# Kernel optimization log

Hardware: AMD Instinct MI355X
Metric: run time of the kernel (lower is better)

Reference implementation:

```python
import jax, jax.numpy as jnp
import numpy as np

HEAD_DIM = 128
PROJ_DIM = 64


def setup_inputs() -> dict:
    key = jax.random.key(0)
    kq, kk, kv, kr = jax.random.split(key, 4)
    B, H, NQ, NKV = 1, 16, 2048, 4096
    Q = jax.random.normal(kq, (B, H, NQ, HEAD_DIM), dtype=jnp.float32)
    K = jax.random.normal(kk, (B, H, NKV, HEAD_DIM), dtype=jnp.float32)
    V = jax.random.normal(kv, (B, H, NKV, HEAD_DIM), dtype=jnp.float32)
    # R ~ N(0,1) / sqrt(proj_dim), as in the torch __init__
    R = jax.random.normal(kr, (HEAD_DIM, PROJ_DIM), dtype=jnp.float32) / (PROJ_DIM ** 0.5)
    return {"Q": Q, "K": K, "V": V, "R": R}


def reference(Q, K, V, R):
    proj_dim = R.shape[-1]
    scale = 1.0 / (proj_dim ** 0.5)
    # Project Q and K into the random-projection space: [B,H,N,proj_dim]
    Q_proj = jnp.einsum('bhnd,dp->bhnp', Q, R)
    K_proj = jnp.einsum('bhmd,dp->bhmp', K, R)
    # scores: [B,H,NQ,NKV]
    scores = jnp.einsum('bhnp,bhmp->bhnm', Q_proj, K_proj) * scale
    weights = jax.nn.softmax(scores, axis=-1)
    # output: [B,H,NQ,head_dim]
    return jnp.einsum('bhnm,bhmd->bhnd', weights, V)
```

## Files before the change

kernel.cpp:

```cpp
#include <hip/hip_runtime.h>

#define HEADS 16
#define NQ    2048
#define NKV   4096
#define DH    128
#define PDIM  64

typedef __bf16 bf16_t;
typedef bf16_t bf16x8 __attribute__((ext_vector_type(8)));
typedef bf16_t bf16x4 __attribute__((ext_vector_type(4)));
typedef bf16_t bf16x2 __attribute__((ext_vector_type(2)));
typedef float  f32x4  __attribute__((ext_vector_type(4)));
typedef float  f32x16 __attribute__((ext_vector_type(16)));
typedef int    i32x4  __attribute__((ext_vector_type(4)));

typedef __attribute__((address_space(3))) unsigned int       lds_u32;
typedef __attribute__((address_space(1))) const unsigned int glb_u32;

__device__ __forceinline__ void dma16(const void* g, void* l) {
  __builtin_amdgcn_global_load_lds((glb_u32*)g, (lds_u32*)l, 16, 0, 0);
}

__global__ __launch_bounds__(256) void proj_kernel(
    const float* __restrict__ Q, const float* __restrict__ K,
    const float* __restrict__ R, bf16_t* __restrict__ Qp, bf16_t* __restrict__ Kp)
{
  __shared__ bf16_t sY[4][16 * 72];
  const int tid  = threadIdx.x;
  const int wave = tid >> 6, lane = tid & 63;
  const int n16  = lane & 15, quad = lane >> 4;

  bf16x8 bfr[4][4];
#pragma unroll
  for (int nt = 0; nt < 4; ++nt) {
    const int n = nt * 16 + n16;
#pragma unroll
    for (int kk = 0; kk < 4; ++kk) {
      const int k0 = kk * 32 + quad * 8;
      bf16x8 b;
#pragma unroll
      for (int j = 0; j < 8; ++j) b[j] = (bf16_t)R[(k0 + j) * PDIM + n];
      bfr[nt][kk] = b;
    }
  }

  const long rowblock = (long)blockIdx.x * 256 + wave * 64;
  const long qrows = (long)HEADS * NQ;

#pragma unroll 1
  for (int t = 0; t < 4; ++t) {
    const long r0 = rowblock + t * 16;
    const float* X; bf16_t* Y; float scale; long xrow;
    if (r0 < qrows) { X = Q; Y = Qp; scale = 0.18033688011112042f; xrow = r0; }
    else            { X = K; Y = Kp; scale = 1.0f;                 xrow = r0 - qrows; }

    const float* xp = X + (xrow + n16) * DH;
    bf16x8 a[4];
#pragma unroll
    for (int kk = 0; kk < 4; ++kk) {
      const int k0 = kk * 32 + quad * 8;
      f32x4 x0 = *(const f32x4*)(xp + k0);
      f32x4 x1 = *(const f32x4*)(xp + k0 + 4);
      bf16x8 av;
#pragma unroll
      for (int j = 0; j < 4; ++j) { av[j] = (bf16_t)(x0[j] * scale); av[4 + j] = (bf16_t)(x1[j] * scale); }
      a[kk] = av;
    }
    bf16_t* sy = sY[wave];
#pragma unroll
    for (int nt = 0; nt < 4; ++nt) {
      f32x4 acc = {0.f, 0.f, 0.f, 0.f};
#pragma unroll
      for (int kk = 0; kk < 4; ++kk)
        acc = __builtin_amdgcn_mfma_f32_16x16x32_bf16(a[kk], bfr[nt][kk], acc, 0, 0, 0);
#pragma unroll
      for (int r = 0; r < 4; ++r)
        sy[(quad * 4 + r) * 72 + nt * 16 + n16] = (bf16_t)acc[r];
    }
    const int row = lane >> 2, cg = lane & 3;
    bf16x8 w0 = *(const bf16x8*)(&sy[row * 72 + cg * 16]);
    bf16x8 w1 = *(const bf16x8*)(&sy[row * 72 + cg * 16 + 8]);
    *(bf16x8*)(Y + (xrow + row) * PDIM + cg * 16)     = w0;
    *(bf16x8*)(Y + (xrow + row) * PDIM + cg * 16 + 8) = w1;
  }
}

__global__ __launch_bounds__(256) void vtrans_kernel(
    const float* __restrict__ V, bf16_t* __restrict__ Vt)
{
  __shared__ float sF[64 * 129];
  const int tid = threadIdx.x;
  const int h = blockIdx.y, jt = blockIdx.x;
  const float* vp = V + ((long)h * NKV + jt * 64) * DH;
#pragma unroll
  for (int rep = 0; rep < 8; ++rep) {
    const int slot = tid + rep * 256;
    const int j = slot >> 5, c4 = (slot & 31) * 4;
    f32x4 v = *(const f32x4*)(vp + j * DH + c4);
    float* dst = &sF[j * 129 + c4];
    dst[0] = v[0]; dst[1] = v[1]; dst[2] = v[2]; dst[3] = v[3];
  }
  __syncthreads();
  bf16_t* op = Vt + (long)h * DH * NKV + jt * 64;
#pragma unroll
  for (int rep = 0; rep < 4; ++rep) {
    const int slot = tid + rep * 256;
    const int d = slot >> 3, j8 = (slot & 7) * 8;
    bf16x8 w;
#pragma unroll
    for (int jj = 0; jj < 8; ++jj) w[jj] = (bf16_t)sF[(j8 + jj) * 129 + d];
    *(bf16x8*)(op + (long)d * NKV + j8) = w;
  }
}

__global__ __launch_bounds__(128, 2) void flash_kernel(
    const bf16_t* __restrict__ Qp, const bf16_t* __restrict__ Kp,
    const bf16_t* __restrict__ Vt, bf16_t* __restrict__ Opart,
    float* __restrict__ Lpart, float* __restrict__ Out,
    int splits, int iters)
{
  __shared__ char smem[24576];
  bf16_t* sK = (bf16_t*)smem;
  bf16_t* sV = (bf16_t*)(smem + 8192);

  const int tid  = threadIdx.x;
  const int wave = tid >> 6, lane = tid & 63;
  const int l31  = lane & 31, h = lane >> 5;

  const int head = blockIdx.x & 15;
  const int qt   = (blockIdx.x >> 4) & 15;
  const int sp   = blockIdx.x >> 8;

  const int qbase = qt * 128 + wave * 64;
  const int kv0   = sp * (64 * iters);

  bf16x8 qf[2][4];
#pragma unroll
  for (int qsub = 0; qsub < 2; ++qsub)
#pragma unroll
    for (int k = 0; k < 4; ++k)
      qf[qsub][k] = *(const bf16x8*)(Qp + ((long)head * NQ + qbase + qsub * 32 + l31) * PDIM
                                     + k * 16 + h * 8);

  f32x16 o[2][4] = {};
  float rsum[2] = {0.f, 0.f};

  const bf16_t* kpH = Kp + (long)head * NKV * PDIM;
  const bf16_t* vtH = Vt + (long)head * DH * NKV;

  const int sw = ((lane & 7) ^ ((lane >> 3) & 7)) * 8;
  const int r8 = lane >> 3;

  for (int t = 0; t < iters; ++t) {
    const int kvb = kv0 + t * 64;
    __syncthreads();
    if (wave == 0) {
#pragma unroll
      for (int i = 0; i < 8; ++i)
        dma16(kpH + (long)(kvb + i * 8 + r8) * PDIM + sw, smem + i * 1024);
#pragma unroll
      for (int i = 0; i < 4; ++i)
        dma16(vtH + (long)(i * 8 + r8) * NKV + kvb + sw, smem + 8192 + i * 1024);
    } else {
#pragma unroll
      for (int i = 4; i < 16; ++i)
        dma16(vtH + (long)(i * 8 + r8) * NKV + kvb + sw, smem + 8192 + i * 1024);
    }
    __syncthreads();

#pragma unroll
    for (int s = 0; s < 2; ++s) {
      int bfr[2][2][4];
#pragma unroll
      for (int qsub = 0; qsub < 2; ++qsub) {
        f32x16 sc = {};
        const int r = s * 32 + l31;
#pragma unroll
        for (int k = 0; k < 4; ++k) {
          const int c = 2 * k + h;
          const bf16x8 a = *(const bf16x8*)(sK + r * 64 + ((c ^ (r & 7)) * 8));
          sc = __builtin_amdgcn_mfma_f32_32x32x16_bf16(a, qf[qsub][k], sc, 0, 0, 0);
        }
        int pk[4][2];
#pragma unroll
        for (int rg = 0; rg < 4; ++rg) {
          const float p0 = __builtin_amdgcn_exp2f(sc[rg * 4 + 0]);
          const float p1 = __builtin_amdgcn_exp2f(sc[rg * 4 + 1]);
          const float p2 = __builtin_amdgcn_exp2f(sc[rg * 4 + 2]);
          const float p3 = __builtin_amdgcn_exp2f(sc[rg * 4 + 3]);
          rsum[qsub] += (p0 + p1) + (p2 + p3);
          union { bf16x2 v; int i; } u0, u1;
          u0.v = bf16x2{(bf16_t)p0, (bf16_t)p1};
          u1.v = bf16x2{(bf16_t)p2, (bf16_t)p3};
          pk[rg][0] = u0.i; pk[rg][1] = u1.i;
        }
#pragma unroll
        for (int cl = 0; cl < 2; ++cl) {
          const int e00 = __shfl_xor(pk[2 * cl][0], 32);
          const int e01 = __shfl_xor(pk[2 * cl][1], 32);
          const int e10 = __shfl_xor(pk[2 * cl + 1][0], 32);
          const int e11 = __shfl_xor(pk[2 * cl + 1][1], 32);
          bfr[qsub][cl][0] = h ? e10 : pk[2 * cl][0];
          bfr[qsub][cl][1] = h ? e11 : pk[2 * cl][1];
          bfr[qsub][cl][2] = h ? pk[2 * cl + 1][0] : e00;
          bfr[qsub][cl][3] = h ? pk[2 * cl + 1][1] : e01;
        }
      }
#pragma unroll
      for (int dsub = 0; dsub < 4; ++dsub) {
        const int r = dsub * 32 + l31;
#pragma unroll
        for (int cl = 0; cl < 2; ++cl) {
          const int c = 2 * (2 * s + cl) + h;
          const bf16x8 va = *(const bf16x8*)(sV + r * 64 + ((c ^ (r & 7)) * 8));
#pragma unroll
          for (int qsub = 0; qsub < 2; ++qsub) {
            union { i32x4 i; bf16x8 v; } pb;
            pb.i = i32x4{bfr[qsub][cl][0], bfr[qsub][cl][1],
                         bfr[qsub][cl][2], bfr[qsub][cl][3]};
            o[qsub][dsub] = __builtin_amdgcn_mfma_f32_32x32x16_bf16(va, pb.v, o[qsub][dsub], 0, 0, 0);
          }
        }
      }
    }
  }

  __syncthreads();
  bf16_t* myT = (bf16_t*)(smem + wave * 8704);
#pragma unroll
  for (int qsub = 0; qsub < 2; ++qsub) {
    const float lsum = rsum[qsub] + __shfl_xor(rsum[qsub], 32);
    const float scale = (splits > 1) ? 1.0f : (1.0f / lsum);
#pragma unroll
    for (int dsub = 0; dsub < 4; ++dsub)
#pragma unroll
      for (int rg = 0; rg < 4; ++rg) {
        bf16x4 w = { (bf16_t)(o[qsub][dsub][rg * 4 + 0] * scale),
                     (bf16_t)(o[qsub][dsub][rg * 4 + 1] * scale),
                     (bf16_t)(o[qsub][dsub][rg * 4 + 2] * scale),
                     (bf16_t)(o[qsub][dsub][rg * 4 + 3] * scale) };
        *(bf16x4*)(myT + l31 * 136 + dsub * 32 + rg * 8 + h * 4) = w;
      }
    const int qglob = qbase + qsub * 32;
#pragma unroll
    for (int j = 0; j < 8; ++j) {
      const int ql = j * 4 + (lane >> 4);
      bf16x8 v = *(const bf16x8*)(myT + ql * 136 + (lane & 15) * 8);
      if (splits > 1) {
        *(bf16x8*)(Opart + (((long)sp * HEADS + head) * NQ + qglob + ql) * DH + (lane & 15) * 8) = v;
      } else {
        float* op = Out + ((long)head * NQ + qglob + ql) * DH + (lane & 15) * 8;
        f32x4 a = {(float)v[0], (float)v[1], (float)v[2], (float)v[3]};
        f32x4 b = {(float)v[4], (float)v[5], (float)v[6], (float)v[7]};
        *(f32x4*)op = a; *(f32x4*)(op + 4) = b;
      }
    }
    if (splits > 1 && h == 0)
      Lpart[((long)sp * HEADS + head) * NQ + qglob + l31] = lsum;
  }
}

__global__ __launch_bounds__(256) void combine_kernel(
    const bf16_t* __restrict__ Opart, const float* __restrict__ Lpart,
    float* __restrict__ Out)
{
  const long idx = (long)blockIdx.x * 256 + threadIdx.x;
  const int  d8  = (int)(idx & 15);
  const long hq  = idx >> 4;
  float l = 0.f;
  float acc[8];
#pragma unroll
  for (int j = 0; j < 8; ++j) acc[j] = 0.f;
#pragma unroll
  for (int s = 0; s < 4; ++s) {
    l += Lpart[s * (long)(HEADS * NQ) + hq];
    bf16x8 v = *(const bf16x8*)(Opart + (s * (long)(HEADS * NQ) + hq) * DH + d8 * 8);
#pragma unroll
    for (int j = 0; j < 8; ++j) acc[j] += (float)v[j];
  }
  const float inv = 1.f / l;
  f32x4 o0 = { acc[0] * inv, acc[1] * inv, acc[2] * inv, acc[3] * inv };
  f32x4 o1 = { acc[4] * inv, acc[5] * inv, acc[6] * inv, acc[7] * inv };
  float* op = Out + hq * DH + d8 * 8;
  *(f32x4*)(op)     = o0;
  *(f32x4*)(op + 4) = o1;
}

extern "C" void kernel_launch(void* const* d_in, const int* in_sizes, int n_in,
                              void* d_out, int out_size, void* d_ws, size_t ws_size,
                              hipStream_t stream)
{
  const float* Q = (const float*)d_in[0];
  const float* K = (const float*)d_in[1];
  const float* V = (const float*)d_in[2];
  const float* R = (const float*)d_in[3];
  float* Out = (float*)d_out;

  char* ws = (char*)d_ws;
  bf16_t* Qp = (bf16_t*)(ws);
  bf16_t* Kp = (bf16_t*)(ws + (size_t)(4  << 20));
  bf16_t* Vt = (bf16_t*)(ws + (size_t)(12 << 20));
  bf16_t* Opart = (bf16_t*)(ws + (size_t)(28 << 20));
  float*  Lpart = (float*)(ws + (size_t)(60 << 20));

  const size_t need4 = (size_t)(60 << 20) + 4ull * HEADS * NQ * sizeof(float);
  const int splits = (ws_size >= need4) ? 4 : 1;
  const int iters  = NKV / (64 * splits);

  proj_kernel<<<384, 256, 0, stream>>>(Q, K, R, Qp, Kp);
  vtrans_kernel<<<dim3(64, 16), 256, 0, stream>>>(V, Vt);
  flash_kernel<<<splits * 256, 128, 0, stream>>>(Qp, Kp, Vt, Opart, Lpart, Out,
                                                 splits, iters);
  if (splits == 4)
    combine_kernel<<<2048, 256, 0, stream>>>(Opart, Lpart, Out);
}
```

Before: 203.6 us.

## Double-buffer K/V tiles, merge prep kernels, use three uneven KV splits

```diff
diff --git a/kernel.cpp b/kernel.cpp
--- a/kernel.cpp
+++ b/kernel.cpp
@@ -21,107 +21,105 @@
   __builtin_amdgcn_global_load_lds((glb_u32*)g, (lds_u32*)l, 16, 0, 0);
 }
 
-__global__ __launch_bounds__(256) void proj_kernel(
+__global__ __launch_bounds__(256) void prep_kernel(
     const float* __restrict__ Q, const float* __restrict__ K,
-    const float* __restrict__ R, bf16_t* __restrict__ Qp, bf16_t* __restrict__ Kp)
+    const float* __restrict__ V, const float* __restrict__ R,
+    bf16_t* __restrict__ Qp, bf16_t* __restrict__ Kp, bf16_t* __restrict__ Vt)
 {
-  __shared__ bf16_t sY[4][16 * 72];
-  const int tid  = threadIdx.x;
-  const int wave = tid >> 6, lane = tid & 63;
-  const int n16  = lane & 15, quad = lane >> 4;
-
-  bf16x8 bfr[4][4];
-#pragma unroll
-  for (int nt = 0; nt < 4; ++nt) {
-    const int n = nt * 16 + n16;
-#pragma unroll
-    for (int kk = 0; kk < 4; ++kk) {
-      const int k0 = kk * 32 + quad * 8;
-      bf16x8 b;
-#pragma unroll
-      for (int j = 0; j < 8; ++j) b[j] = (bf16_t)R[(k0 + j) * PDIM + n];
-      bfr[nt][kk] = b;
-    }
-  }
-
-  const long rowblock = (long)blockIdx.x * 256 + wave * 64;
-  const long qrows = (long)HEADS * NQ;
+  __shared__ char smem_raw[33024 * 4 > 36864 ? 33024 * 4 / 1 : 36864];
+  const int tid = threadIdx.x;
+
+  if (blockIdx.x < 384) {
+    bf16_t* sY = (bf16_t*)smem_raw;
+    const int wave = tid >> 6, lane = tid & 63;
+    const int n16  = lane & 15, quad = lane >> 4;
+
+    bf16x8 bfr[4][4];
+#pragma unroll
+    for (int nt = 0; nt < 4; ++nt) {
+      const int n = nt * 16 + n16;
+#pragma unroll
+      for (int kk = 0; kk < 4; ++kk) {
+        const int k0 = kk * 32 + quad * 8;
+        bf16x8 b;
+#pragma unroll
+        for (int j = 0; j < 8; ++j) b[j] = (bf16_t)R[(k0 + j) * PDIM + n];
+        bfr[nt][kk] = b;
+      }
+    }
+
+    const long rowblock = (long)blockIdx.x * 256 + wave * 64;
+    const long qrows = (long)HEADS * NQ;
 
 #pragma unroll 1
-  for (int t = 0; t < 4; ++t) {
-    const long r0 = rowblock + t * 16;
-    const float* X; bf16_t* Y; float scale; long xrow;
-    if (r0 < qrows) { X = Q; Y = Qp; scale = 0.18033688011112042f; xrow = r0; }
-    else            { X = K; Y = Kp; scale = 1.0f;                 xrow = r0 - qrows; }
-
-    const float* xp = X + (xrow + n16) * DH;
-    bf16x8 a[4];
-#pragma unroll
-    for (int kk = 0; kk < 4; ++kk) {
-      const int k0 = kk * 32 + quad * 8;
-      f32x4 x0 = *(const f32x4*)(xp + k0);
-      f32x4 x1 = *(const f32x4*)(xp + k0 + 4);
-      bf16x8 av;
-#pragma unroll
-      for (int j = 0; j < 4; ++j) { av[j] = (bf16_t)(x0[j] * scale); av[4 + j] = (bf16_t)(x1[j] * scale); }
-      a[kk] = av;
-    }
-    bf16_t* sy = sY[wave];
-#pragma unroll
-    for (int nt = 0; nt < 4; ++nt) {
-      f32x4 acc = {0.f, 0.f, 0.f, 0.f};
-#pragma unroll
-      for (int kk = 0; kk < 4; ++kk)
-        acc = __builtin_amdgcn_mfma_f32_16x16x32_bf16(a[kk], bfr[nt][kk], acc, 0, 0, 0);
-#pragma unroll
-      for (int r = 0; r < 4; ++r)
-        sy[(quad * 4 + r) * 72 + nt * 16 + n16] = (bf16_t)acc[r];
-    }
-    const int row = lane >> 2, cg = lane & 3;
-    bf16x8 w0 = *(const bf16x8*)(&sy[row * 72 + cg * 16]);
-    bf16x8 w1 = *(const bf16x8*)(&sy[row * 72 + cg * 16 + 8]);
-    *(bf16x8*)(Y + (xrow + row) * PDIM + cg * 16)     = w0;
-    *(bf16x8*)(Y + (xrow + row) * PDIM + cg * 16 + 8) = w1;
-  }
-}
-
-__global__ __launch_bounds__(256) void vtrans_kernel(
-    const float* __restrict__ V, bf16_t* __restrict__ Vt)
-{
-  __shared__ float sF[64 * 129];
-  const int tid = threadIdx.x;
-  const int h = blockIdx.y, jt = blockIdx.x;
-  const float* vp = V + ((long)h * NKV + jt * 64) * DH;
-#pragma unroll
-  for (int rep = 0; rep < 8; ++rep) {
-    const int slot = tid + rep * 256;
-    const int j = slot >> 5, c4 = (slot & 31) * 4;
-    f32x4 v = *(const f32x4*)(vp + j * DH + c4);
-    float* dst = &sF[j * 129 + c4];
-    dst[0] = v[0]; dst[1] = v[1]; dst[2] = v[2]; dst[3] = v[3];
-  }
-  __syncthreads();
-  bf16_t* op = Vt + (long)h * DH * NKV + jt * 64;
-#pragma unroll
-  for (int rep = 0; rep < 4; ++rep) {
-    const int slot = tid + rep * 256;
-    const int d = slot >> 3, j8 = (slot & 7) * 8;
-    bf16x8 w;
-#pragma unroll
-    for (int jj = 0; jj < 8; ++jj) w[jj] = (bf16_t)sF[(j8 + jj) * 129 + d];
-    *(bf16x8*)(op + (long)d * NKV + j8) = w;
+    for (int t = 0; t < 4; ++t) {
+      const long r0 = rowblock + t * 16;
+      const float* X; bf16_t* Y; float scale; long xrow;
+      if (r0 < qrows) { X = Q; Y = Qp; scale = 0.18033688011112042f; xrow = r0; }
+      else            { X = K; Y = Kp; scale = 1.0f;                 xrow = r0 - qrows; }
+
+      const float* xp = X + (xrow + n16) * DH;
+      bf16x8 a[4];
+#pragma unroll
+      for (int kk = 0; kk < 4; ++kk) {
+        const int k0 = kk * 32 + quad * 8;
+        f32x4 x0 = *(const f32x4*)(xp + k0);
+        f32x4 x1 = *(const f32x4*)(xp + k0 + 4);
+        bf16x8 av;
+#pragma unroll
+        for (int j = 0; j < 4; ++j) { av[j] = (bf16_t)(x0[j] * scale); av[4 + j] = (bf16_t)(x1[j] * scale); }
+        a[kk] = av;
+      }
+      bf16_t* sy = sY + wave * (16 * 72);
+#pragma unroll
+      for (int nt = 0; nt < 4; ++nt) {
+        f32x4 acc = {0.f, 0.f, 0.f, 0.f};
+#pragma unroll
+        for (int kk = 0; kk < 4; ++kk)
+          acc = __builtin_amdgcn_mfma_f32_16x16x32_bf16(a[kk], bfr[nt][kk], acc, 0, 0, 0);
+#pragma unroll
+        for (int r = 0; r < 4; ++r)
+          sy[(quad * 4 + r) * 72 + nt * 16 + n16] = (bf16_t)acc[r];
+      }
+      const int row = lane >> 2, cg = lane & 3;
+      bf16x8 w0 = *(const bf16x8*)(&sy[row * 72 + cg * 16]);
+      bf16x8 w1 = *(const bf16x8*)(&sy[row * 72 + cg * 16 + 8]);
+      *(bf16x8*)(Y + (xrow + row) * PDIM + cg * 16)     = w0;
+      *(bf16x8*)(Y + (xrow + row) * PDIM + cg * 16 + 8) = w1;
+    }
+  } else {
+    float* sF = (float*)smem_raw;
+    const int bid = blockIdx.x - 384;
+    const int h = bid >> 6, jt = bid & 63;
+    const float* vp = V + ((long)h * NKV + jt * 64) * DH;
+#pragma unroll
+    for (int rep = 0; rep < 8; ++rep) {
+      const int slot = tid + rep * 256;
+      const int j = slot >> 5, c4 = (slot & 31) * 4;
+      f32x4 v = *(const f32x4*)(vp + j * DH + c4);
+      float* dst = &sF[j * 129 + c4];
+      dst[0] = v[0]; dst[1] = v[1]; dst[2] = v[2]; dst[3] = v[3];
+    }
+    __syncthreads();
+    bf16_t* op = Vt + (long)h * DH * NKV + jt * 64;
+#pragma unroll
+    for (int rep = 0; rep < 4; ++rep) {
+      const int slot = tid + rep * 256;
+      const int d = slot >> 3, j8 = (slot & 7) * 8;
+      bf16x8 w;
+#pragma unroll
+      for (int jj = 0; jj < 8; ++jj) w[jj] = (bf16_t)sF[(j8 + jj) * 129 + d];
+      *(bf16x8*)(op + (long)d * NKV + j8) = w;
+    }
   }
 }
 
 __global__ __launch_bounds__(128, 2) void flash_kernel(
     const bf16_t* __restrict__ Qp, const bf16_t* __restrict__ Kp,
     const bf16_t* __restrict__ Vt, bf16_t* __restrict__ Opart,
-    float* __restrict__ Lpart, float* __restrict__ Out,
-    int splits, int iters)
+    float* __restrict__ Lpart, float* __restrict__ Out, int splits)
 {
-  __shared__ char smem[24576];
-  bf16_t* sK = (bf16_t*)smem;
-  bf16_t* sV = (bf16_t*)(smem + 8192);
+  __shared__ char smem[49152];
 
   const int tid  = threadIdx.x;
   const int wave = tid >> 6, lane = tid & 63;
@@ -132,7 +130,33 @@
   const int sp   = blockIdx.x >> 8;
 
   const int qbase = qt * 128 + wave * 64;
-  const int kv0   = sp * (64 * iters);
+  int n_t, t0;
+  if (splits == 3) { n_t = (sp == 0) ? 22 : 21; t0 = (sp == 0) ? 0 : 22 + 21 * (sp - 1); }
+  else             { n_t = 64; t0 = 0; }
+
+  const bf16_t* kpH = Kp + (long)head * NKV * PDIM;
+  const bf16_t* vtH = Vt + (long)head * DH * NKV;
+
+  const int sw = ((lane & 7) ^ ((lane >> 3) & 7)) * 8;
+  const int r8 = lane >> 3;
+
+  auto stage = [&](int t, char* buf) {
+    const int kvb = (t0 + t) * 64;
+    if (wave == 0) {
+#pragma unroll
+      for (int i = 0; i < 8; ++i)
+        dma16(kpH + (long)(kvb + i * 8 + r8) * PDIM + sw, buf + i * 1024);
+#pragma unroll
+      for (int i = 0; i < 4; ++i)
+        dma16(vtH + (long)(i * 8 + r8) * NKV + kvb + sw, buf + 8192 + i * 1024);
+    } else {
+#pragma unroll
+      for (int i = 4; i < 16; ++i)
+        dma16(vtH + (long)(i * 8 + r8) * NKV + kvb + sw, buf + 8192 + i * 1024);
+    }
+  };
+
+  stage(0, smem);
 
   bf16x8 qf[2][4];
 #pragma unroll
@@ -145,28 +169,13 @@
   f32x16 o[2][4] = {};
   float rsum[2] = {0.f, 0.f};
 
-  const bf16_t* kpH = Kp + (long)head * NKV * PDIM;
-  const bf16_t* vtH = Vt + (long)head * DH * NKV;
-
-  const int sw = ((lane & 7) ^ ((lane >> 3) & 7)) * 8;
-  const int r8 = lane >> 3;
-
-  for (int t = 0; t < iters; ++t) {
-    const int kvb = kv0 + t * 64;
+  for (int t = 0; t < n_t; ++t) {
     __syncthreads();
-    if (wave == 0) {
-#pragma unroll
-      for (int i = 0; i < 8; ++i)
-        dma16(kpH + (long)(kvb + i * 8 + r8) * PDIM + sw, smem + i * 1024);
-#pragma unroll
-      for (int i = 0; i < 4; ++i)
-        dma16(vtH + (long)(i * 8 + r8) * NKV + kvb + sw, smem + 8192 + i * 1024);
-    } else {
-#pragma unroll
-      for (int i = 4; i < 16; ++i)
-        dma16(vtH + (long)(i * 8 + r8) * NKV + kvb + sw, smem + 8192 + i * 1024);
-    }
-    __syncthreads();
+    if (t + 1 < n_t) stage(t + 1, smem + ((t + 1) & 1) * 24576);
+
+    char* cur = smem + (t & 1) * 24576;
+    bf16_t* sK = (bf16_t*)cur;
+    bf16_t* sV = (bf16_t*)(cur + 8192);
 
 #pragma unroll
     for (int s = 0; s < 2; ++s) {
@@ -262,7 +271,7 @@
 
 __global__ __launch_bounds__(256) void combine_kernel(
     const bf16_t* __restrict__ Opart, const float* __restrict__ Lpart,
-    float* __restrict__ Out)
+    float* __restrict__ Out, int splits)
 {
   const long idx = (long)blockIdx.x * 256 + threadIdx.x;
   const int  d8  = (int)(idx & 15);
@@ -271,8 +280,8 @@
   float acc[8];
 #pragma unroll
   for (int j = 0; j < 8; ++j) acc[j] = 0.f;
-#pragma unroll
-  for (int s = 0; s < 4; ++s) {
+#pragma unroll 1
+  for (int s = 0; s < splits; ++s) {
     l += Lpart[s * (long)(HEADS * NQ) + hq];
     bf16x8 v = *(const bf16x8*)(Opart + (s * (long)(HEADS * NQ) + hq) * DH + d8 * 8);
 #pragma unroll
@@ -301,16 +310,13 @@
   bf16_t* Kp = (bf16_t*)(ws + (size_t)(4  << 20));
   bf16_t* Vt = (bf16_t*)(ws + (size_t)(12 << 20));
   bf16_t* Opart = (bf16_t*)(ws + (size_t)(28 << 20));
-  float*  Lpart = (float*)(ws + (size_t)(60 << 20));
-
-  const size_t need4 = (size_t)(60 << 20) + 4ull * HEADS * NQ * sizeof(float);
-  const int splits = (ws_size >= need4) ? 4 : 1;
-  const int iters  = NKV / (64 * splits);
-
-  proj_kernel<<<384, 256, 0, stream>>>(Q, K, R, Qp, Kp);
-  vtrans_kernel<<<dim3(64, 16), 256, 0, stream>>>(V, Vt);
-  flash_kernel<<<splits * 256, 128, 0, stream>>>(Qp, Kp, Vt, Opart, Lpart, Out,
-                                                 splits, iters);
-  if (splits == 4)
-    combine_kernel<<<2048, 256, 0, stream>>>(Opart, Lpart, Out);
-}
+  float*  Lpart = (float*)(ws + (size_t)(52 << 20));
+
+  const size_t need3 = (size_t)(52 << 20) + 3ull * HEADS * NQ * sizeof(float);
+  const int splits = (ws_size >= need3) ? 3 : 1;
+
+  prep_kernel<<<1408, 256, 0, stream>>>(Q, K, V, R, Qp, Kp, Vt);
+  flash_kernel<<<splits * 256, 128, 0, stream>>>(Qp, Kp, Vt, Opart, Lpart, Out, splits);
+  if (splits == 3)
+    combine_kernel<<<2048, 256, 0, stream>>>(Opart, Lpart, Out, splits);
+}
```

Measured after the change: 262.9 us. 1.29x slower.

## Merge Q/K projection and V transpose into one prep kernel

Applied to the files above, without the earlier changes.

```diff
diff --git a/kernel.cpp b/kernel.cpp
--- a/kernel.cpp
+++ b/kernel.cpp
@@ -21,14 +21,54 @@
   __builtin_amdgcn_global_load_lds((glb_u32*)g, (lds_u32*)l, 16, 0, 0);
 }
 
-__global__ __launch_bounds__(256) void proj_kernel(
+__global__ __launch_bounds__(256) void prep_kernel(
     const float* __restrict__ Q, const float* __restrict__ K,
-    const float* __restrict__ R, bf16_t* __restrict__ Qp, bf16_t* __restrict__ Kp)
+    const float* __restrict__ V, const float* __restrict__ R,
+    bf16_t* __restrict__ Qp, bf16_t* __restrict__ Kp, bf16_t* __restrict__ Vt)
 {
+  __shared__ float  sF[64 * 132];
   __shared__ bf16_t sY[4][16 * 72];
-  const int tid  = threadIdx.x;
+  const int tid = threadIdx.x;
+  const int bid = blockIdx.x;
+
+  const int isQ = (bid < 512);
+  const int isK = (bid >= 512) && (bid < 1536);
+
+  const float* src;
+  long row0;
+  if (isQ)      { src = Q; row0 = (long)bid * 64; }
+  else if (isK) { src = K; row0 = (long)(bid - 512) * 64; }
+  else          { src = V; row0 = (long)(bid - 1536) * 64; }
+  const float* tp = src + row0 * DH;
+#pragma unroll
+  for (int rep = 0; rep < 8; ++rep) {
+    const int slot = tid + rep * 256;
+    const int j = slot >> 5, c4 = (slot & 31) * 4;
+    f32x4 v = *(const f32x4*)(tp + j * DH + c4);
+    *(f32x4*)(&sF[j * 132 + c4]) = v;
+  }
+  __syncthreads();
+
+  if (!isQ && !isK) {
+    const int vb = bid - 1536;
+    const int h = vb >> 6, jt = vb & 63;
+    bf16_t* op = Vt + (long)h * DH * NKV + jt * 64;
+#pragma unroll
+    for (int rep = 0; rep < 4; ++rep) {
+      const int slot = tid + rep * 256;
+      const int d = slot >> 3, j8 = (slot & 7) * 8;
+      bf16x8 w;
+#pragma unroll
+      for (int jj = 0; jj < 8; ++jj) w[jj] = (bf16_t)sF[(j8 + jj) * 132 + d];
+      *(bf16x8*)(op + (long)d * NKV + j8) = w;
+    }
+    return;
+  }
+
   const int wave = tid >> 6, lane = tid & 63;
   const int n16  = lane & 15, quad = lane >> 4;
+  const float scale = isQ ? 0.18033688011112042f : 1.0f;
+  bf16_t* Y = isQ ? Qp : Kp;
 
   bf16x8 bfr[4][4];
 #pragma unroll
@@ -44,73 +84,36 @@
     }
   }
 
-  const long rowblock = (long)blockIdx.x * 256 + wave * 64;
-  const long qrows = (long)HEADS * NQ;
-
-#pragma unroll 1
-  for (int t = 0; t < 4; ++t) {
-    const long r0 = rowblock + t * 16;
-    const float* X; bf16_t* Y; float scale; long xrow;
-    if (r0 < qrows) { X = Q; Y = Qp; scale = 0.18033688011112042f; xrow = r0; }
-    else            { X = K; Y = Kp; scale = 1.0f;                 xrow = r0 - qrows; }
-
-    const float* xp = X + (xrow + n16) * DH;
-    bf16x8 a[4];
-#pragma unroll
-    for (int kk = 0; kk < 4; ++kk) {
-      const int k0 = kk * 32 + quad * 8;
-      f32x4 x0 = *(const f32x4*)(xp + k0);
-      f32x4 x1 = *(const f32x4*)(xp + k0 + 4);
-      bf16x8 av;
-#pragma unroll
-      for (int j = 0; j < 4; ++j) { av[j] = (bf16_t)(x0[j] * scale); av[4 + j] = (bf16_t)(x1[j] * scale); }
-      a[kk] = av;
-    }
-    bf16_t* sy = sY[wave];
-#pragma unroll
-    for (int nt = 0; nt < 4; ++nt) {
-      f32x4 acc = {0.f, 0.f, 0.f, 0.f};
-#pragma unroll
-      for (int kk = 0; kk < 4; ++kk)
-        acc = __builtin_amdgcn_mfma_f32_16x16x32_bf16(a[kk], bfr[nt][kk], acc, 0, 0, 0);
-#pragma unroll
-      for (int r = 0; r < 4; ++r)
-        sy[(quad * 4 + r) * 72 + nt * 16 + n16] = (bf16_t)acc[r];
-    }
-    const int row = lane >> 2, cg = lane & 3;
-    bf16x8 w0 = *(const bf16x8*)(&sy[row * 72 + cg * 16]);
-    bf16x8 w1 = *(const bf16x8*)(&sy[row * 72 + cg * 16 + 8]);
-    *(bf16x8*)(Y + (xrow + row) * PDIM + cg * 16)     = w0;
-    *(bf16x8*)(Y + (xrow + row) * PDIM + cg * 16 + 8) = w1;
-  }
-}
-
-__global__ __launch_bounds__(256) void vtrans_kernel(
-    const float* __restrict__ V, bf16_t* __restrict__ Vt)
-{
-  __shared__ float sF[64 * 129];
-  const int tid = threadIdx.x;
-  const int h = blockIdx.y, jt = blockIdx.x;
-  const float* vp = V + ((long)h * NKV + jt * 64) * DH;
-#pragma unroll
-  for (int rep = 0; rep < 8; ++rep) {
-    const int slot = tid + rep * 256;
-    const int j = slot >> 5, c4 = (slot & 31) * 4;
-    f32x4 v = *(const f32x4*)(vp + j * DH + c4);
-    float* dst = &sF[j * 129 + c4];
-    dst[0] = v[0]; dst[1] = v[1]; dst[2] = v[2]; dst[3] = v[3];
-  }
-  __syncthreads();
-  bf16_t* op = Vt + (long)h * DH * NKV + jt * 64;
-#pragma unroll
-  for (int rep = 0; rep < 4; ++rep) {
-    const int slot = tid + rep * 256;
-    const int d = slot >> 3, j8 = (slot & 7) * 8;
-    bf16x8 w;
-#pragma unroll
-    for (int jj = 0; jj < 8; ++jj) w[jj] = (bf16_t)sF[(j8 + jj) * 129 + d];
-    *(bf16x8*)(op + (long)d * NKV + j8) = w;
-  }
+  const int arow = wave * 16 + n16;
+  bf16x8 a[4];
+#pragma unroll
+  for (int kk = 0; kk < 4; ++kk) {
+    const int k0 = kk * 32 + quad * 8;
+    f32x4 x0 = *(const f32x4*)(&sF[arow * 132 + k0]);
+    f32x4 x1 = *(const f32x4*)(&sF[arow * 132 + k0 + 4]);
+    bf16x8 av;
+#pragma unroll
+    for (int j = 0; j < 4; ++j) { av[j] = (bf16_t)(x0[j] * scale); av[4 + j] = (bf16_t)(x1[j] * scale); }
+    a[kk] = av;
+  }
+
+  bf16_t* sy = sY[wave];
+#pragma unroll
+  for (int nt = 0; nt < 4; ++nt) {
+    f32x4 acc = {0.f, 0.f, 0.f, 0.f};
+#pragma unroll
+    for (int kk = 0; kk < 4; ++kk)
+      acc = __builtin_amdgcn_mfma_f32_16x16x32_bf16(a[kk], bfr[nt][kk], acc, 0, 0, 0);
+#pragma unroll
+    for (int r = 0; r < 4; ++r)
+      sy[(quad * 4 + r) * 72 + nt * 16 + n16] = (bf16_t)acc[r];
+  }
+  const long xrow = row0 + wave * 16;
+  const int row = lane >> 2, cg = lane & 3;
+  bf16x8 w0 = *(const bf16x8*)(&sy[row * 72 + cg * 16]);
+  bf16x8 w1 = *(const bf16x8*)(&sy[row * 72 + cg * 16 + 8]);
+  *(bf16x8*)(Y + (xrow + row) * PDIM + cg * 16)     = w0;
+  *(bf16x8*)(Y + (xrow + row) * PDIM + cg * 16 + 8) = w1;
 }
 
 __global__ __launch_bounds__(128, 2) void flash_kernel(
@@ -307,8 +310,7 @@
   const int splits = (ws_size >= need4) ? 4 : 1;
   const int iters  = NKV / (64 * splits);
 
-  proj_kernel<<<384, 256, 0, stream>>>(Q, K, R, Qp, Kp);
-  vtrans_kernel<<<dim3(64, 16), 256, 0, stream>>>(V, Vt);
+  prep_kernel<<<2560, 256, 0, stream>>>(Q, K, V, R, Qp, Kp, Vt);
   flash_kernel<<<splits * 256, 128, 0, stream>>>(Qp, Kp, Vt, Opart, Lpart, Out,
                                                  splits, iters);
   if (splits == 4)
```

After: 197.0 us. 3.3% less time.
